# Kernel tuning notes

Measured on AMD Instinct MI355X. Metric: run time of the kernel, lower is better.

The kernel has to match this reference:

```python
import jax, jax.numpy as jnp
import numpy as np

NUM_BLOCKS = 3
NUM_CLUSTER = [16, 32, 64]


def _conv(x, w, b):
    # 1x1 conv2d + ReLU (BN folded to identity, eval-mode default stats): x [B,d,N], w [o,d], b [o]
    return jax.nn.relu(jnp.einsum('bdn,od->bon', x, w) + b[None, :, None])


def _segment_pool(feat, idx, nc):
    # Faithful single-pass version of pooling_block: per-cluster max over N,
    # rebroadcast to every node of that cluster. feat [B,d,N], idx [B,N] int.
    B, d, N = feat.shape
    seg = (idx + jnp.arange(B, dtype=idx.dtype)[:, None] * nc).reshape(-1)  # [B*N]
    flat = feat.transpose(0, 2, 1).reshape(B * N, d)
    mx = jax.ops.segment_max(flat, seg, num_segments=B * nc)  # [B*nc, d]
    return mx[seg].reshape(B, N, d).transpose(0, 2, 1)  # [B,d,N]


def setup_inputs() -> dict:
    key = jax.random.key(0)
    ks = jax.random.split(key, 16)
    B, N, K = 8, 16384, 28
    s = 0.05
    f32 = jnp.float32
    return {
        'x': jax.random.normal(ks[0], (B, N, K), f32),
        'clusters': jax.random.randint(ks[1], (NUM_BLOCKS, B, N), 0, min(NUM_CLUSTER), dtype=jnp.int32),
        'w_in': jax.random.normal(ks[2], (256, K), f32) * s,
        'b_in': jnp.zeros((256,), f32),
        'w1': jax.random.normal(ks[3], (NUM_BLOCKS, 64, 256), f32) * s,
        'b1': jnp.zeros((NUM_BLOCKS, 64), f32),
        'w2': jax.random.normal(ks[4], (NUM_BLOCKS, 128, 64), f32) * s,
        'b2': jnp.zeros((NUM_BLOCKS, 128), f32),
        'w3': jax.random.normal(ks[5], (NUM_BLOCKS, 128, 128), f32) * s,
        'b3': jnp.zeros((NUM_BLOCKS, 128), f32),
        'w_out1': jax.random.normal(ks[6], (128, 256), f32) * s,
        'b_out1': jnp.zeros((128,), f32),
        'w_out2': jax.random.normal(ks[7], (128, 128), f32) * s,
        'b_out2': jnp.zeros((128,), f32),
    }


def reference(x, clusters, w_in, b_in, w1, b1, w2, b2, w3, b3, w_out1, b_out1, w_out2, b_out2):
    # mlp_in: conv2d kernel [1,28] contracts the feature width -> [B,256,N]
    f = jax.nn.relu(jnp.einsum('bnk,ok->bon', x, w_in) + b_in[None, :, None])
    for i in range(NUM_BLOCKS):
        f = _conv(f, w1[i], b1[i])          # [B,64,N]
        f = _conv(f, w2[i], b2[i])          # [B,128,N]
        pool = _segment_pool(f, clusters[i], NUM_CLUSTER[i])  # [B,128,N]
        f3 = _conv(f, w3[i], b3[i])         # [B,128,N]
        f = jnp.concatenate([f3, pool], axis=1)  # [B,256,N]
    o1 = _conv(f, w_out1, b_out1)           # [B,128,N]
    o2 = _conv(o1, w_out2, b_out2)          # [B,128,N]
    out_max = o2.max(axis=2)                # global max pool over N
    B, d = out_max.shape
    return out_max.reshape(B, d, 1, 1)
```

## Files before the change

kernel.cpp:

```cpp
#include <hip/hip_runtime.h>
#include <hip/hip_cooperative_groups.h>


namespace cg = cooperative_groups;

typedef __attribute__((ext_vector_type(8))) short bf16x8;
typedef __attribute__((ext_vector_type(4))) float f32x4;
typedef __attribute__((ext_vector_type(4))) unsigned u32x4;
typedef __attribute__((ext_vector_type(4))) float f32x4v;

#define MFMA16(a, b, c) __builtin_amdgcn_mfma_f32_16x16x32_bf16((a), (b), (c), 0, 0, 0)

#define TPB 512
#define PT 64
#define NPTS 131072
#define NC 16
#define TILES 4
#define NBLK 512

#define FSB 136
#define ASB 72
#define XSB 40

#define U_F256 0
#define U_W1_0 16
#define U_W2_0 48
#define U_W3_0 64
#define U_W1_1 96
#define U_W2_1 112
#define U_W3_1 128
#define U_W1_2 160
#define U_W2_2 176
#define U_W3_2 192
#define U_O1   224
#define U_O2   256
#define N_UNITS 288

__device__ __forceinline__ float agent_ldf(const float* p) {
  return __hip_atomic_load(p, __ATOMIC_RELAXED, __HIP_MEMORY_SCOPE_AGENT);
}
__device__ __forceinline__ unsigned agent_ldu(const unsigned* p) {
  return __hip_atomic_load(p, __ATOMIC_RELAXED, __HIP_MEMORY_SCOPE_AGENT);
}
__device__ __forceinline__ void agent_stf(float* p, float v) {
  __hip_atomic_store(p, v, __ATOMIC_RELAXED, __HIP_MEMORY_SCOPE_AGENT);
}

__device__ __forceinline__ f32x4 relu4(f32x4 a) {
#pragma unroll
  for (int r = 0; r < 4; ++r) a[r] = fmaxf(a[r], 0.f);
  return a;
}

__device__ __forceinline__ bf16x8 afrag(const short* plane, int stride, int mt, int ks) {
  const int lane = threadIdx.x & 63;
  return *reinterpret_cast<const bf16x8*>(
      plane + (mt * 16 + (lane & 15)) * stride + ks * 32 + (lane >> 4) * 8);
}

__device__ __forceinline__ void bfrag(const unsigned* __restrict__ arena, int unit,
                                      bf16x8& h, bf16x8& l) {
  const bf16x8* p = reinterpret_cast<const bf16x8*>(
      arena + ((size_t)unit * 64 + (threadIdx.x & 63)) * 8);
  h = p[0];
  l = p[1];
}

__device__ __forceinline__ void store_planes(short* hp, short* lp, int stride,
                                             int mt, int n, f32x4 d) {
  const int m0 = mt * 16 + ((threadIdx.x & 63) >> 4) * 4;
#pragma unroll
  for (int r = 0; r < 4; ++r) {
    unsigned uv = __float_as_uint(d[r]);
    unsigned hm = uv & 0xFFFF0000u;
    float lo = d[r] - __uint_as_float(hm);
    hp[(m0 + r) * stride + n] = (short)(hm >> 16);
    lp[(m0 + r) * stride + n] = (short)(__float_as_uint(lo) >> 16);
  }
}

__device__ __forceinline__ void stage_f3(const unsigned* __restrict__ f3g, int tile0,
                                         short* Fhi, short* Flo, int tid) {
  const u32x4* src = reinterpret_cast<const u32x4*>(f3g + (size_t)tile0 * 128);
#pragma unroll
  for (int rr = 0; rr < 4; ++rr) {
    const int idx = rr * TPB + tid;
    const u32x4 p = __builtin_nontemporal_load(src + idx);
    const int pt = idx >> 5, c4 = (idx & 31) * 4;
    uint2 hd, ld;
    hd.x = (p.y & 0xFFFF0000u) | (p.x >> 16);
    hd.y = (p.w & 0xFFFF0000u) | (p.z >> 16);
    ld.x = (p.y << 16) | (p.x & 0xFFFFu);
    ld.y = (p.w << 16) | (p.z & 0xFFFFu);
    *reinterpret_cast<uint2*>(&Fhi[pt * FSB + c4]) = hd;
    *reinterpret_cast<uint2*>(&Flo[pt * FSB + c4]) = ld;
  }
}

__device__ __forceinline__ void write_f3(unsigned* __restrict__ f3g, int tile0,
                                         const short* Fhi, const short* Flo, int tid) {
  u32x4* dst = reinterpret_cast<u32x4*>(f3g + (size_t)tile0 * 128);
#pragma unroll
  for (int rr = 0; rr < 4; ++rr) {
    const int idx = rr * TPB + tid;
    const int pt = idx >> 5, c4 = (idx & 31) * 4;
    const uint2 hd = *reinterpret_cast<const uint2*>(&Fhi[pt * FSB + c4]);
    const uint2 ld = *reinterpret_cast<const uint2*>(&Flo[pt * FSB + c4]);
    u32x4 p;
    p.x = (hd.x << 16) | (ld.x & 0xFFFFu);
    p.y = (hd.x & 0xFFFF0000u) | (ld.x >> 16);
    p.z = (hd.y << 16) | (ld.y & 0xFFFFu);
    p.w = (hd.y & 0xFFFF0000u) | (ld.y >> 16);
    __builtin_nontemporal_store(p, dst + idx);
  }
}

__device__ __forceinline__ void unpack_cf(const u32x4 (&c)[4], short* Fhi, short* Flo,
                                          int tid) {
#pragma unroll
  for (int rr = 0; rr < 4; ++rr) {
    const int idx = rr * TPB + tid;
    const int pt = idx >> 5, c4 = (idx & 31) * 4;
    const u32x4 p = c[rr];
    uint2 hd, ld;
    hd.x = (p.y & 0xFFFF0000u) | (p.x >> 16);
    hd.y = (p.w & 0xFFFF0000u) | (p.z >> 16);
    ld.x = (p.y << 16) | (p.x & 0xFFFFu);
    ld.y = (p.w << 16) | (p.z & 0xFFFFu);
    *reinterpret_cast<uint2*>(&Fhi[pt * FSB + c4]) = hd;
    *reinterpret_cast<uint2*>(&Flo[pt * FSB + c4]) = ld;
  }
}

__device__ __forceinline__ void pack_cf(u32x4 (&c)[4], const short* Fhi, const short* Flo,
                                        int tid) {
#pragma unroll
  for (int rr = 0; rr < 4; ++rr) {
    const int idx = rr * TPB + tid;
    const int pt = idx >> 5, c4 = (idx & 31) * 4;
    const uint2 hd = *reinterpret_cast<const uint2*>(&Fhi[pt * FSB + c4]);
    const uint2 ld = *reinterpret_cast<const uint2*>(&Flo[pt * FSB + c4]);
    u32x4 p;
    p.x = (hd.x << 16) | (ld.x & 0xFFFFu);
    p.y = (hd.x & 0xFFFF0000u) | (ld.x >> 16);
    p.z = (hd.y << 16) | (ld.y & 0xFFFFu);
    p.w = (hd.y & 0xFFFF0000u) | (ld.y >> 16);
    c[rr] = p;
  }
}

__global__ void __launch_bounds__(64) prep_frags(
    const float* __restrict__ w_in, const float* __restrict__ w1,
    const float* __restrict__ w2, const float* __restrict__ w3,
    const float* __restrict__ wo1, const float* __restrict__ wo2,
    unsigned* __restrict__ arena) {
  const int unit = blockIdx.x;
  const int lane = threadIdx.x;
  const float* W; int KS, Klog, rs, u;
  if (unit < U_W1_0)      { W = w_in;                   u = unit - U_F256; KS = 1; Klog = 28;  rs = 28;  }
  else if (unit < U_W2_0) { W = w1;                     u = unit - U_W1_0; KS = 8; Klog = 256; rs = 256; }
  else if (unit < U_W3_0) { W = w2;                     u = unit - U_W2_0; KS = 2; Klog = 64;  rs = 64;  }
  else if (unit < U_W1_1) { W = w3;                     u = unit - U_W3_0; KS = 4; Klog = 128; rs = 128; }
  else if (unit < U_W2_1) { W = w1 + 64 * 256;          u = unit - U_W1_1; KS = 4; Klog = 128; rs = 256; }
  else if (unit < U_W3_1) { W = w2 + 128 * 64;          u = unit - U_W2_1; KS = 2; Klog = 64;  rs = 64;  }
  else if (unit < U_W1_2) { W = w3 + 128 * 128;         u = unit - U_W3_1; KS = 4; Klog = 128; rs = 128; }
  else if (unit < U_W2_2) { W = w1 + 2 * 64 * 256;      u = unit - U_W1_2; KS = 4; Klog = 128; rs = 256; }
  else if (unit < U_W3_2) { W = w2 + 2 * 128 * 64;      u = unit - U_W2_2; KS = 2; Klog = 64;  rs = 64;  }
  else if (unit < U_O1)   { W = w3 + 2 * 128 * 128;     u = unit - U_W3_2; KS = 4; Klog = 128; rs = 128; }
  else if (unit < U_O2)   { W = wo1;                    u = unit - U_O1;   KS = 4; Klog = 128; rs = 256; }
  else                    { W = wo2;                    u = unit - U_O2;   KS = 4; Klog = 128; rs = 128; }
  const int nt = u / KS, ks = u % KS;
  const int n = nt * 16 + (lane & 15);
  const int k0 = ks * 32 + (lane >> 4) * 8;
  unsigned hiD[4], loD[4];
#pragma unroll
  for (int d = 0; d < 4; ++d) {
    unsigned hu[2], lu[2];
#pragma unroll
    for (int e = 0; e < 2; ++e) {
      const int k = k0 + d * 2 + e;
      float v = (k < Klog) ? W[(size_t)n * rs + k] : 0.f;
      unsigned uv = __float_as_uint(v);
      unsigned hm = uv & 0xFFFF0000u;
      float lo = v - __uint_as_float(hm);
      hu[e] = hm >> 16;
      lu[e] = __float_as_uint(lo) >> 16;
    }
    hiD[d] = hu[0] | (hu[1] << 16);
    loD[d] = lu[0] | (lu[1] << 16);
  }
  unsigned* dst = arena + ((size_t)unit * 64 + lane) * 8;
  *reinterpret_cast<uint4*>(dst)     = make_uint4(hiD[0], hiD[1], hiD[2], hiD[3]);
  *reinterpret_cast<uint4*>(dst + 4) = make_uint4(loD[0], loD[1], loD[2], loD[3]);
}


template<int O>
__global__ void __launch_bounds__(1024) pool_reduce_kern(
    const unsigned* __restrict__ part, const float* __restrict__ W,
    const float* __restrict__ bias, float* __restrict__ poolc_g) {
  __shared__ float pfL[2048];
  __shared__ float Wl[O * 129];
  const int tid = threadIdx.x;
  const int b = blockIdx.x;
  for (int i = tid; i < 2048; i += 1024) pfL[i] = __uint_as_float(part[b * 2048 + i]);
  for (int i = tid; i < O * 128; i += 1024) {
    const int o = i >> 7, k = i & 127;
    Wl[o * 129 + k] = W[o * 256 + 128 + k];
  }
  __syncthreads();
  constexpr int SH = (O == 64) ? 6 : 7;
  for (int e = tid; e < O * 16; e += 1024) {
    const int o = e & (O - 1);
    const int cl = e >> SH;
    float s = bias[o];
    const float* wr = &Wl[o * 129];
    const float* pr = &pfL[cl];
#pragma unroll 4
    for (int k = 0; k < 128; ++k) s = fmaf(wr[k], pr[k * 16], s);
    poolc_g[(size_t)b * (O * 16) + o * 16 + cl] = s;
  }
}

__global__ void __launch_bounds__(TPB, 4) k0_kern(
    const float* __restrict__ x, const int* __restrict__ cls,
    const float* __restrict__ b_in, const float* __restrict__ b1,
    const float* __restrict__ b2, const float* __restrict__ b3,
    const unsigned* __restrict__ arena,
    unsigned* __restrict__ f3g, unsigned* __restrict__ part0) {
  __shared__ short Fhi[PT * FSB], Flo[PT * FSB];
  __shared__ short XA[PT * ASB * 2];
  __shared__ unsigned pool_s[128 * NC];
  short* Xhi = XA;  short* Xlo = XA + PT * XSB;
  short* Ahi = XA;  short* Alo = XA + PT * ASB;
  const int tid = threadIdx.x;
  const int lane = tid & 63, w = tid >> 6, l15 = lane & 15, quad = lane >> 4;
  const int b = blockIdx.x >> 6;
  const int Nt1 = w & 3, mh = w >> 2;
  for (int i = tid; i < 128 * NC; i += TPB) pool_s[i] = 0u;

  float biH[2];
#pragma unroll
  for (int c = 0; c < 2; ++c) biH[c] = b_in[c * 128 + w * 16 + l15];
  const float b1H = b1[Nt1 * 16 + l15];
  const float b2H = b2[w * 16 + l15];
  const float b3H = b3[w * 16 + l15];
  const int n1 = Nt1 * 16 + l15;
  const int n2 = w * 16 + l15;
  const int xpt = (tid < 448) ? tid / 7 : 0;
  const int xc4 = (tid < 448) ? (tid - xpt * 7) * 4 : 0;

  for (int t = 0; t < TILES; ++t) {
    const int tile0 = (blockIdx.x * TILES + t) * PT;
    if (tid < 448) {
      const f32x4v v = __builtin_nontemporal_load(
          reinterpret_cast<const f32x4v*>(x + (size_t)(tile0 + xpt) * 28 + xc4));
      unsigned h0 = __float_as_uint(v.x) & 0xFFFF0000u, h1 = __float_as_uint(v.y) & 0xFFFF0000u;
      unsigned h2 = __float_as_uint(v.z) & 0xFFFF0000u, h3 = __float_as_uint(v.w) & 0xFFFF0000u;
      uint2 hd, ld;
      hd.x = (h0 >> 16) | h1;
      hd.y = (h2 >> 16) | h3;
      ld.x = (__float_as_uint(v.x - __uint_as_float(h0)) >> 16) |
             (__float_as_uint(v.y - __uint_as_float(h1)) & 0xFFFF0000u);
      ld.y = (__float_as_uint(v.z - __uint_as_float(h2)) >> 16) |
             (__float_as_uint(v.w - __uint_as_float(h3)) & 0xFFFF0000u);
      *reinterpret_cast<uint2*>(&Xhi[xpt * XSB + xc4]) = hd;
      *reinterpret_cast<uint2*>(&Xlo[xpt * XSB + xc4]) = ld;
    } else {
      const int p = tid - 448;
      *reinterpret_cast<uint2*>(&Xhi[p * XSB + 28]) = make_uint2(0u, 0u);
      *reinterpret_cast<uint2*>(&Xlo[p * XSB + 28]) = make_uint2(0u, 0u);
    }
    int clP[4][4];
#pragma unroll
    for (int Mt = 0; Mt < 4; ++Mt) {
      int4 v = *reinterpret_cast<const int4*>(cls + tile0 + Mt * 16 + quad * 4);
      clP[Mt][0] = v.x; clP[Mt][1] = v.y; clP[Mt][2] = v.z; clP[Mt][3] = v.w;
    }
    __syncthreads();
    f32x4 a1[2];
#pragma unroll
    for (int m = 0; m < 2; ++m) a1[m] = {b1H, b1H, b1H, b1H};
#pragma unroll 1
    for (int c = 0; c < 2; ++c) {
      f32x4 f6[4];
#pragma unroll
      for (int Mt = 0; Mt < 4; ++Mt) f6[Mt] = {biH[c], biH[c], biH[c], biH[c]};
      {
        bf16x8 bh, bl;
        bfrag(arena, U_F256 + c * 8 + w, bh, bl);
#pragma unroll
        for (int Mt = 0; Mt < 4; ++Mt) {
          const bf16x8 xah = afrag(Xhi, XSB, Mt, 0), xal = afrag(Xlo, XSB, Mt, 0);
          f6[Mt] = MFMA16(xal, bh, MFMA16(xah, bl, MFMA16(xah, bh, f6[Mt])));
        }
      }
#pragma unroll
      for (int Mt = 0; Mt < 4; ++Mt)
        store_planes(Fhi, Flo, FSB, Mt, n2, relu4(f6[Mt]));
      __syncthreads();
#pragma unroll
      for (int ks = 0; ks < 4; ++ks) {
        bf16x8 bh, bl;
        bfrag(arena, U_W1_0 + Nt1 * 8 + c * 4 + ks, bh, bl);
#pragma unroll
        for (int m = 0; m < 2; ++m) {
          const bf16x8 ah = afrag(Fhi, FSB, mh * 2 + m, ks), al = afrag(Flo, FSB, mh * 2 + m, ks);
          a1[m] = MFMA16(al, bh, MFMA16(ah, bl, MFMA16(ah, bh, a1[m])));
        }
      }
      if (c == 1) {
#pragma unroll
        for (int m = 0; m < 2; ++m)
          store_planes(Ahi, Alo, ASB, mh * 2 + m, n1, relu4(a1[m]));
      }
      __syncthreads();
    }
    f32x4 f2[4];
#pragma unroll
    for (int Mt = 0; Mt < 4; ++Mt) f2[Mt] = {b2H, b2H, b2H, b2H};
#pragma unroll
    for (int ks = 0; ks < 2; ++ks) {
      bf16x8 bh, bl;
      bfrag(arena, U_W2_0 + w * 2 + ks, bh, bl);
#pragma unroll
      for (int Mt = 0; Mt < 4; ++Mt) {
        const bf16x8 ah = afrag(Ahi, ASB, Mt, ks), al = afrag(Alo, ASB, Mt, ks);
        f2[Mt] = MFMA16(al, bh, MFMA16(ah, bl, MFMA16(ah, bh, f2[Mt])));
      }
    }
#pragma unroll
    for (int Mt = 0; Mt < 4; ++Mt) {
      f32x4 d = relu4(f2[Mt]);
#pragma unroll
      for (int r = 0; r < 4; ++r)
        atomicMax(&pool_s[n2 * NC + clP[Mt][r]], __float_as_uint(d[r]));
      store_planes(Fhi, Flo, FSB, Mt, n2, d);
    }
    __syncthreads();
    f32x4 f3a[4];
#pragma unroll
    for (int Mt = 0; Mt < 4; ++Mt) f3a[Mt] = {b3H, b3H, b3H, b3H};
#pragma unroll
    for (int ks = 0; ks < 4; ++ks) {
      bf16x8 bh, bl;
      bfrag(arena, U_W3_0 + w * 4 + ks, bh, bl);
#pragma unroll
      for (int Mt = 0; Mt < 4; ++Mt) {
        const bf16x8 ah = afrag(Fhi, FSB, Mt, ks), al = afrag(Flo, FSB, Mt, ks);
        f3a[Mt] = MFMA16(al, bh, MFMA16(ah, bl, MFMA16(ah, bh, f3a[Mt])));
      }
    }
    __syncthreads();
#pragma unroll
    for (int Mt = 0; Mt < 4; ++Mt)
      store_planes(Fhi, Flo, FSB, Mt, n2, relu4(f3a[Mt]));
    __syncthreads();
    write_f3(f3g, tile0, Fhi, Flo, tid);
  }
  for (int i = tid; i < 128 * NC; i += TPB)
    atomicMax(&part0[(size_t)b * 2048 + i], pool_s[i]);
}

__global__ void __launch_bounds__(TPB, 4) kmid_kern(
    unsigned* __restrict__ f3g, const unsigned* __restrict__ arena,
    const float* __restrict__ poolc_g, unsigned* __restrict__ part_cur,
    const int* __restrict__ clg, const int* __restrict__ clp,
    const float* __restrict__ b2s, const float* __restrict__ b3s,
    int uW1, int uW2, int uW3) {
  __shared__ short Fhi[PT * FSB], Flo[PT * FSB];
  __shared__ short Ahi[PT * ASB], Alo[PT * ASB];
  __shared__ unsigned pool_s[128 * NC];
  const int tid = threadIdx.x;
  const int lane = tid & 63, w = tid >> 6, l15 = lane & 15, quad = lane >> 4;
  const int b = blockIdx.x >> 6;
  const int Nt1 = w & 3, mh = w >> 2;
  for (int i = tid; i < 128 * NC; i += TPB) pool_s[i] = 0u;
  const float b2H = b2s[w * 16 + l15];
  const float b3H = b3s[w * 16 + l15];
  const int n1 = Nt1 * 16 + l15;
  const int n2 = w * 16 + l15;

  for (int t = 0; t < TILES; ++t) {
    const int tile0 = (blockIdx.x * TILES + t) * PT;
    stage_f3(f3g, tile0, Fhi, Flo, tid);
    int clG[2][4], clP[4][4];
#pragma unroll
    for (int m = 0; m < 2; ++m) {
      int4 v = *reinterpret_cast<const int4*>(clg + tile0 + (mh * 2 + m) * 16 + quad * 4);
      clG[m][0] = v.x; clG[m][1] = v.y; clG[m][2] = v.z; clG[m][3] = v.w;
    }
#pragma unroll
    for (int Mt = 0; Mt < 4; ++Mt) {
      int4 v = *reinterpret_cast<const int4*>(clp + tile0 + Mt * 16 + quad * 4);
      clP[Mt][0] = v.x; clP[Mt][1] = v.y; clP[Mt][2] = v.z; clP[Mt][3] = v.w;
    }
    __syncthreads();
    f32x4 a1[2];
#pragma unroll
    for (int m = 0; m < 2; ++m)
#pragma unroll
      for (int r = 0; r < 4; ++r)
        a1[m][r] = poolc_g[(size_t)b * 1024 + n1 * 16 + clG[m][r]];
#pragma unroll
    for (int ks = 0; ks < 4; ++ks) {
      bf16x8 bh, bl;
      bfrag(arena, uW1 + Nt1 * 4 + ks, bh, bl);
#pragma unroll
      for (int m = 0; m < 2; ++m) {
        const bf16x8 ah = afrag(Fhi, FSB, mh * 2 + m, ks), al = afrag(Flo, FSB, mh * 2 + m, ks);
        a1[m] = MFMA16(al, bh, MFMA16(ah, bl, MFMA16(ah, bh, a1[m])));
      }
    }
#pragma unroll
    for (int m = 0; m < 2; ++m)
      store_planes(Ahi, Alo, ASB, mh * 2 + m, n1, relu4(a1[m]));
    __syncthreads();
    f32x4 f2[4];
#pragma unroll
    for (int Mt = 0; Mt < 4; ++Mt) f2[Mt] = {b2H, b2H, b2H, b2H};
#pragma unroll
    for (int ks = 0; ks < 2; ++ks) {
      bf16x8 bh, bl;
      bfrag(arena, uW2 + w * 2 + ks, bh, bl);
#pragma unroll
      for (int Mt = 0; Mt < 4; ++Mt) {
        const bf16x8 ah = afrag(Ahi, ASB, Mt, ks), al = afrag(Alo, ASB, Mt, ks);
        f2[Mt] = MFMA16(al, bh, MFMA16(ah, bl, MFMA16(ah, bh, f2[Mt])));
      }
    }
#pragma unroll
    for (int Mt = 0; Mt < 4; ++Mt) {
      f32x4 d = relu4(f2[Mt]);
#pragma unroll
      for (int r = 0; r < 4; ++r)
        atomicMax(&pool_s[n2 * NC + clP[Mt][r]], __float_as_uint(d[r]));
      store_planes(Fhi, Flo, FSB, Mt, n2, d);
    }
    __syncthreads();
    f32x4 f3a[4];
#pragma unroll
    for (int Mt = 0; Mt < 4; ++Mt) f3a[Mt] = {b3H, b3H, b3H, b3H};
#pragma unroll
    for (int ks = 0; ks < 4; ++ks) {
      bf16x8 bh, bl;
      bfrag(arena, uW3 + w * 4 + ks, bh, bl);
#pragma unroll
      for (int Mt = 0; Mt < 4; ++Mt) {
        const bf16x8 ah = afrag(Fhi, FSB, Mt, ks), al = afrag(Flo, FSB, Mt, ks);
        f3a[Mt] = MFMA16(al, bh, MFMA16(ah, bl, MFMA16(ah, bh, f3a[Mt])));
      }
    }
    __syncthreads();
#pragma unroll
    for (int Mt = 0; Mt < 4; ++Mt)
      store_planes(Fhi, Flo, FSB, Mt, n2, relu4(f3a[Mt]));
    __syncthreads();
    write_f3(f3g, tile0, Fhi, Flo, tid);
    __syncthreads();
  }
  for (int i = tid; i < 128 * NC; i += TPB)
    atomicMax(&part_cur[(size_t)b * 2048 + i], pool_s[i]);
}

__global__ void __launch_bounds__(TPB, 4) k3_kern(
    const unsigned* __restrict__ f3g, const unsigned* __restrict__ arena,
    const float* __restrict__ poolco_g, const int* __restrict__ clg,
    const float* __restrict__ bo2, unsigned* __restrict__ out) {
  __shared__ short Fhi[PT * FSB], Flo[PT * FSB];
  const int tid = threadIdx.x;
  const int lane = tid & 63, w = tid >> 6, l15 = lane & 15, quad = lane >> 4;
  const int b = blockIdx.x >> 6;
  const float bo2H = bo2[w * 16 + l15];
  const int n2 = w * 16 + l15;
  float omax = 0.f;

  for (int t = 0; t < TILES; ++t) {
    const int tile0 = (blockIdx.x * TILES + t) * PT;
    stage_f3(f3g, tile0, Fhi, Flo, tid);
    int clA[4][4];
#pragma unroll
    for (int Mt = 0; Mt < 4; ++Mt) {
      int4 v = *reinterpret_cast<const int4*>(clg + tile0 + Mt * 16 + quad * 4);
      clA[Mt][0] = v.x; clA[Mt][1] = v.y; clA[Mt][2] = v.z; clA[Mt][3] = v.w;
    }
    __syncthreads();
    f32x4 o1a[4];
#pragma unroll
    for (int Mt = 0; Mt < 4; ++Mt)
#pragma unroll
      for (int r = 0; r < 4; ++r)
        o1a[Mt][r] = poolco_g[(size_t)b * 2048 + n2 * 16 + clA[Mt][r]];
#pragma unroll
    for (int ks = 0; ks < 4; ++ks) {
      bf16x8 bh, bl;
      bfrag(arena, U_O1 + w * 4 + ks, bh, bl);
#pragma unroll
      for (int Mt = 0; Mt < 4; ++Mt) {
        const bf16x8 ah = afrag(Fhi, FSB, Mt, ks), al = afrag(Flo, FSB, Mt, ks);
        o1a[Mt] = MFMA16(al, bh, MFMA16(ah, bl, MFMA16(ah, bh, o1a[Mt])));
      }
    }
    __syncthreads();
#pragma unroll
    for (int Mt = 0; Mt < 4; ++Mt)
      store_planes(Fhi, Flo, FSB, Mt, n2, relu4(o1a[Mt]));
    __syncthreads();
    f32x4 o2a[4];
#pragma unroll
    for (int Mt = 0; Mt < 4; ++Mt) o2a[Mt] = {bo2H, bo2H, bo2H, bo2H};
#pragma unroll
    for (int ks = 0; ks < 4; ++ks) {
      bf16x8 bh, bl;
      bfrag(arena, U_O2 + w * 4 + ks, bh, bl);
#pragma unroll
      for (int Mt = 0; Mt < 4; ++Mt) {
        const bf16x8 ah = afrag(Fhi, FSB, Mt, ks), al = afrag(Flo, FSB, Mt, ks);
        o2a[Mt] = MFMA16(al, bh, MFMA16(ah, bl, MFMA16(ah, bh, o2a[Mt])));
      }
    }
#pragma unroll
    for (int Mt = 0; Mt < 4; ++Mt) {
      f32x4 d = relu4(o2a[Mt]);
      omax = fmaxf(omax, fmaxf(fmaxf(d[0], d[1]), fmaxf(d[2], d[3])));
    }
    __syncthreads();
  }
  omax = fmaxf(omax, __shfl_xor(omax, 16));
  omax = fmaxf(omax, __shfl_xor(omax, 32));
  if (lane < 16)
    atomicMax(&out[b * 128 + w * 16 + lane], __float_as_uint(omax));
}


__device__ __forceinline__ void poolc_phase(const unsigned* __restrict__ part,
                                            const float* __restrict__ W,
                                            const float* __restrict__ bias,
                                            float* __restrict__ poolc,
                                            int O, int tid, int wg) {
  const int b = wg >> 3, j = wg & 7;
  const int per = O >> 3;
  const int njobs = per * 16;
  if (tid < njobs) {
    const int o = j * per + (tid >> 4);
    const int cl = tid & 15;
    float s = bias[o];
    const float* wr = W + (size_t)o * 256 + 128;
    const unsigned* pr = part + b * 2048 + cl;
#pragma unroll 4
    for (int k = 0; k < 128; ++k) s = fmaf(wr[k], __uint_as_float(agent_ldu(pr + k * 16)), s);
    agent_stf(poolc + (size_t)b * (O * 16) + o * 16 + cl, s);
  }
}

__device__ __forceinline__ void stage0_body(
    u32x4 (&cf)[TILES][4],
    const float* __restrict__ x, const int* __restrict__ cls,
    const float* __restrict__ b_in, const float* __restrict__ b1,
    const float* __restrict__ b2, const float* __restrict__ b3,
    const unsigned* __restrict__ arena, unsigned* __restrict__ part0,
    short* Fhi, short* Flo, short* XA, unsigned* pool_s,
    int tid, int wg, int b) {
  short* Xhi = XA;  short* Xlo = XA + PT * XSB;
  short* Ahi = XA;  short* Alo = XA + PT * ASB;
  const int lane = tid & 63, w = tid >> 6, l15 = lane & 15, quad = lane >> 4;
  const int Nt1 = w & 3, mh = w >> 2;
  for (int i = tid; i < 128 * NC; i += TPB) pool_s[i] = 0u;

  float biH[2];
#pragma unroll
  for (int c = 0; c < 2; ++c) biH[c] = b_in[c * 128 + w * 16 + l15];
  const float b1H = b1[Nt1 * 16 + l15];
  const float b2H = b2[w * 16 + l15];
  const float b3H = b3[w * 16 + l15];
  const int n1 = Nt1 * 16 + l15;
  const int n2 = w * 16 + l15;
  const int xpt = (tid < 448) ? tid / 7 : 0;
  const int xc4 = (tid < 448) ? (tid - xpt * 7) * 4 : 0;

#pragma unroll
  for (int t = 0; t < TILES; ++t) {
    const int tile0 = (wg * TILES + t) * PT;
    if (tid < 448) {
      const f32x4v v = __builtin_nontemporal_load(
          reinterpret_cast<const f32x4v*>(x + (size_t)(tile0 + xpt) * 28 + xc4));
      unsigned h0 = __float_as_uint(v.x) & 0xFFFF0000u, h1 = __float_as_uint(v.y) & 0xFFFF0000u;
      unsigned h2 = __float_as_uint(v.z) & 0xFFFF0000u, h3 = __float_as_uint(v.w) & 0xFFFF0000u;
      uint2 hd, ld;
      hd.x = (h0 >> 16) | h1;
      hd.y = (h2 >> 16) | h3;
      ld.x = (__float_as_uint(v.x - __uint_as_float(h0)) >> 16) |
             (__float_as_uint(v.y - __uint_as_float(h1)) & 0xFFFF0000u);
      ld.y = (__float_as_uint(v.z - __uint_as_float(h2)) >> 16) |
             (__float_as_uint(v.w - __uint_as_float(h3)) & 0xFFFF0000u);
      *reinterpret_cast<uint2*>(&Xhi[xpt * XSB + xc4]) = hd;
      *reinterpret_cast<uint2*>(&Xlo[xpt * XSB + xc4]) = ld;
    } else {
      const int p = tid - 448;
      *reinterpret_cast<uint2*>(&Xhi[p * XSB + 28]) = make_uint2(0u, 0u);
      *reinterpret_cast<uint2*>(&Xlo[p * XSB + 28]) = make_uint2(0u, 0u);
    }
    int clP[4][4];
#pragma unroll
    for (int Mt = 0; Mt < 4; ++Mt) {
      int4 v = *reinterpret_cast<const int4*>(cls + tile0 + Mt * 16 + quad * 4);
      clP[Mt][0] = v.x; clP[Mt][1] = v.y; clP[Mt][2] = v.z; clP[Mt][3] = v.w;
    }
    __syncthreads();
    f32x4 a1[2];
#pragma unroll
    for (int m = 0; m < 2; ++m) a1[m] = {b1H, b1H, b1H, b1H};
#pragma unroll 1
    for (int c = 0; c < 2; ++c) {
      f32x4 f6[4];
#pragma unroll
      for (int Mt = 0; Mt < 4; ++Mt) f6[Mt] = {biH[c], biH[c], biH[c], biH[c]};
      {
        bf16x8 bh, bl;
        bfrag(arena, U_F256 + c * 8 + w, bh, bl);
#pragma unroll
        for (int Mt = 0; Mt < 4; ++Mt) {
          const bf16x8 xah = afrag(Xhi, XSB, Mt, 0), xal = afrag(Xlo, XSB, Mt, 0);
          f6[Mt] = MFMA16(xal, bh, MFMA16(xah, bl, MFMA16(xah, bh, f6[Mt])));
        }
      }
#pragma unroll
      for (int Mt = 0; Mt < 4; ++Mt)
        store_planes(Fhi, Flo, FSB, Mt, n2, relu4(f6[Mt]));
      __syncthreads();
#pragma unroll
      for (int ks = 0; ks < 4; ++ks) {
        bf16x8 bh, bl;
        bfrag(arena, U_W1_0 + Nt1 * 8 + c * 4 + ks, bh, bl);
#pragma unroll
        for (int m = 0; m < 2; ++m) {
          const bf16x8 ah = afrag(Fhi, FSB, mh * 2 + m, ks), al = afrag(Flo, FSB, mh * 2 + m, ks);
          a1[m] = MFMA16(al, bh, MFMA16(ah, bl, MFMA16(ah, bh, a1[m])));
        }
      }
      if (c == 1) {
#pragma unroll
        for (int m = 0; m < 2; ++m)
          store_planes(Ahi, Alo, ASB, mh * 2 + m, n1, relu4(a1[m]));
      }
      __syncthreads();
    }
    f32x4 f2[4];
#pragma unroll
    for (int Mt = 0; Mt < 4; ++Mt) f2[Mt] = {b2H, b2H, b2H, b2H};
#pragma unroll
    for (int ks = 0; ks < 2; ++ks) {
      bf16x8 bh, bl;
      bfrag(arena, U_W2_0 + w * 2 + ks, bh, bl);
#pragma unroll
      for (int Mt = 0; Mt < 4; ++Mt) {
        const bf16x8 ah = afrag(Ahi, ASB, Mt, ks), al = afrag(Alo, ASB, Mt, ks);
        f2[Mt] = MFMA16(al, bh, MFMA16(ah, bl, MFMA16(ah, bh, f2[Mt])));
      }
    }
#pragma unroll
    for (int Mt = 0; Mt < 4; ++Mt) {
      f32x4 d = relu4(f2[Mt]);
#pragma unroll
      for (int r = 0; r < 4; ++r)
        atomicMax(&pool_s[n2 * NC + clP[Mt][r]], __float_as_uint(d[r]));
      store_planes(Fhi, Flo, FSB, Mt, n2, d);
    }
    __syncthreads();
    f32x4 f3a[4];
#pragma unroll
    for (int Mt = 0; Mt < 4; ++Mt) f3a[Mt] = {b3H, b3H, b3H, b3H};
#pragma unroll
    for (int ks = 0; ks < 4; ++ks) {
      bf16x8 bh, bl;
      bfrag(arena, U_W3_0 + w * 4 + ks, bh, bl);
#pragma unroll
      for (int Mt = 0; Mt < 4; ++Mt) {
        const bf16x8 ah = afrag(Fhi, FSB, Mt, ks), al = afrag(Flo, FSB, Mt, ks);
        f3a[Mt] = MFMA16(al, bh, MFMA16(ah, bl, MFMA16(ah, bh, f3a[Mt])));
      }
    }
    __syncthreads();
#pragma unroll
    for (int Mt = 0; Mt < 4; ++Mt)
      store_planes(Fhi, Flo, FSB, Mt, n2, relu4(f3a[Mt]));
    __syncthreads();
    pack_cf(cf[t], Fhi, Flo, tid);
  }
  for (int i = tid; i < 128 * NC; i += TPB)
    atomicMax(&part0[(size_t)b * 2048 + i], pool_s[i]);
}

__device__ __forceinline__ void mid_body(
    u32x4 (&cf)[TILES][4], const unsigned* __restrict__ arena,
    const float* __restrict__ poolc_g, unsigned* __restrict__ part_cur,
    const int* __restrict__ clg, const int* __restrict__ clp,
    const float* __restrict__ b2s, const float* __restrict__ b3s,
    int uW1, int uW2, int uW3,
    short* Fhi, short* Flo, short* Ahi, short* Alo, unsigned* pool_s,
    int tid, int wg, int b) {
  const int lane = tid & 63, w = tid >> 6, l15 = lane & 15, quad = lane >> 4;
  const int Nt1 = w & 3, mh = w >> 2;
  for (int i = tid; i < 128 * NC; i += TPB) pool_s[i] = 0u;
  const float b2H = b2s[w * 16 + l15];
  const float b3H = b3s[w * 16 + l15];
  const int n1 = Nt1 * 16 + l15;
  const int n2 = w * 16 + l15;

#pragma unroll
  for (int t = 0; t < TILES; ++t) {
    const int tile0 = (wg * TILES + t) * PT;
    unpack_cf(cf[t], Fhi, Flo, tid);
    int clG[2][4], clP[4][4];
#pragma unroll
    for (int m = 0; m < 2; ++m) {
      int4 v = *reinterpret_cast<const int4*>(clg + tile0 + (mh * 2 + m) * 16 + quad * 4);
      clG[m][0] = v.x; clG[m][1] = v.y; clG[m][2] = v.z; clG[m][3] = v.w;
    }
#pragma unroll
    for (int Mt = 0; Mt < 4; ++Mt) {
      int4 v = *reinterpret_cast<const int4*>(clp + tile0 + Mt * 16 + quad * 4);
      clP[Mt][0] = v.x; clP[Mt][1] = v.y; clP[Mt][2] = v.z; clP[Mt][3] = v.w;
    }
    __syncthreads();
    f32x4 a1[2];
#pragma unroll
    for (int m = 0; m < 2; ++m)
#pragma unroll
      for (int r = 0; r < 4; ++r)
        a1[m][r] = agent_ldf(poolc_g + (size_t)b * 1024 + n1 * 16 + clG[m][r]);
#pragma unroll
    for (int ks = 0; ks < 4; ++ks) {
      bf16x8 bh, bl;
      bfrag(arena, uW1 + Nt1 * 4 + ks, bh, bl);
#pragma unroll
      for (int m = 0; m < 2; ++m) {
        const bf16x8 ah = afrag(Fhi, FSB, mh * 2 + m, ks), al = afrag(Flo, FSB, mh * 2 + m, ks);
        a1[m] = MFMA16(al, bh, MFMA16(ah, bl, MFMA16(ah, bh, a1[m])));
      }
    }
#pragma unroll
    for (int m = 0; m < 2; ++m)
      store_planes(Ahi, Alo, ASB, mh * 2 + m, n1, relu4(a1[m]));
    __syncthreads();
    f32x4 f2[4];
#pragma unroll
    for (int Mt = 0; Mt < 4; ++Mt) f2[Mt] = {b2H, b2H, b2H, b2H};
#pragma unroll
    for (int ks = 0; ks < 2; ++ks) {
      bf16x8 bh, bl;
      bfrag(arena, uW2 + w * 2 + ks, bh, bl);
#pragma unroll
      for (int Mt = 0; Mt < 4; ++Mt) {
        const bf16x8 ah = afrag(Ahi, ASB, Mt, ks), al = afrag(Alo, ASB, Mt, ks);
        f2[Mt] = MFMA16(al, bh, MFMA16(ah, bl, MFMA16(ah, bh, f2[Mt])));
      }
    }
#pragma unroll
    for (int Mt = 0; Mt < 4; ++Mt) {
      f32x4 d = relu4(f2[Mt]);
#pragma unroll
      for (int r = 0; r < 4; ++r)
        atomicMax(&pool_s[n2 * NC + clP[Mt][r]], __float_as_uint(d[r]));
      store_planes(Fhi, Flo, FSB, Mt, n2, d);
    }
    __syncthreads();
    f32x4 f3a[4];
#pragma unroll
    for (int Mt = 0; Mt < 4; ++Mt) f3a[Mt] = {b3H, b3H, b3H, b3H};
#pragma unroll
    for (int ks = 0; ks < 4; ++ks) {
      bf16x8 bh, bl;
      bfrag(arena, uW3 + w * 4 + ks, bh, bl);
#pragma unroll
      for (int Mt = 0; Mt < 4; ++Mt) {
        const bf16x8 ah = afrag(Fhi, FSB, Mt, ks), al = afrag(Flo, FSB, Mt, ks);
        f3a[Mt] = MFMA16(al, bh, MFMA16(ah, bl, MFMA16(ah, bh, f3a[Mt])));
      }
    }
    __syncthreads();
#pragma unroll
    for (int Mt = 0; Mt < 4; ++Mt)
      store_planes(Fhi, Flo, FSB, Mt, n2, relu4(f3a[Mt]));
    __syncthreads();
    pack_cf(cf[t], Fhi, Flo, tid);
    __syncthreads();
  }
  for (int i = tid; i < 128 * NC; i += TPB)
    atomicMax(&part_cur[(size_t)b * 2048 + i], pool_s[i]);
}

__device__ __forceinline__ void head_body(
    const u32x4 (&cf)[TILES][4], const unsigned* __restrict__ arena,
    const float* __restrict__ poolco_g, const int* __restrict__ clg,
    const float* __restrict__ bo2, unsigned* __restrict__ out,
    short* Fhi, short* Flo, int tid, int wg, int b) {
  const int lane = tid & 63, w = tid >> 6, l15 = lane & 15, quad = lane >> 4;
  const float bo2H = bo2[w * 16 + l15];
  const int n2 = w * 16 + l15;
  float omax = 0.f;

#pragma unroll
  for (int t = 0; t < TILES; ++t) {
    const int tile0 = (wg * TILES + t) * PT;
    unpack_cf(cf[t], Fhi, Flo, tid);
    int clA[4][4];
#pragma unroll
    for (int Mt = 0; Mt < 4; ++Mt) {
      int4 v = *reinterpret_cast<const int4*>(clg + tile0 + Mt * 16 + quad * 4);
      clA[Mt][0] = v.x; clA[Mt][1] = v.y; clA[Mt][2] = v.z; clA[Mt][3] = v.w;
    }
    __syncthreads();
    f32x4 o1a[4];
#pragma unroll
    for (int Mt = 0; Mt < 4; ++Mt)
#pragma unroll
      for (int r = 0; r < 4; ++r)
        o1a[Mt][r] = agent_ldf(poolco_g + (size_t)b * 2048 + n2 * 16 + clA[Mt][r]);
#pragma unroll
    for (int ks = 0; ks < 4; ++ks) {
      bf16x8 bh, bl;
      bfrag(arena, U_O1 + w * 4 + ks, bh, bl);
#pragma unroll
      for (int Mt = 0; Mt < 4; ++Mt) {
        const bf16x8 ah = afrag(Fhi, FSB, Mt, ks), al = afrag(Flo, FSB, Mt, ks);
        o1a[Mt] = MFMA16(al, bh, MFMA16(ah, bl, MFMA16(ah, bh, o1a[Mt])));
      }
    }
    __syncthreads();
#pragma unroll
    for (int Mt = 0; Mt < 4; ++Mt)
      store_planes(Fhi, Flo, FSB, Mt, n2, relu4(o1a[Mt]));
    __syncthreads();
    f32x4 o2a[4];
#pragma unroll
    for (int Mt = 0; Mt < 4; ++Mt) o2a[Mt] = {bo2H, bo2H, bo2H, bo2H};
#pragma unroll
    for (int ks = 0; ks < 4; ++ks) {
      bf16x8 bh, bl;
      bfrag(arena, U_O2 + w * 4 + ks, bh, bl);
#pragma unroll
      for (int Mt = 0; Mt < 4; ++Mt) {
        const bf16x8 ah = afrag(Fhi, FSB, Mt, ks), al = afrag(Flo, FSB, Mt, ks);
        o2a[Mt] = MFMA16(al, bh, MFMA16(ah, bl, MFMA16(ah, bh, o2a[Mt])));
      }
    }
#pragma unroll
    for (int Mt = 0; Mt < 4; ++Mt) {
      f32x4 d = relu4(o2a[Mt]);
      omax = fmaxf(omax, fmaxf(fmaxf(d[0], d[1]), fmaxf(d[2], d[3])));
    }
    __syncthreads();
  }
  omax = fmaxf(omax, __shfl_xor(omax, 16));
  omax = fmaxf(omax, __shfl_xor(omax, 32));
  if (lane < 16)
    atomicMax(&out[b * 128 + w * 16 + lane], __float_as_uint(omax));
}

struct FusedParams {
  const float* x; const int* cls;
  const float* b_in; const float* b1; const float* b2; const float* b3;
  const float* w1; const float* wo1; const float* bo1; const float* bo2;
  const unsigned* arena;
  unsigned* part0; unsigned* part1; unsigned* part2;
  float* poolc1; float* poolc2; float* poolco;
  unsigned* out;
};

__global__ void __launch_bounds__(TPB, 4) fused_kern(FusedParams P) {
  __shared__ short Fhi[PT * FSB], Flo[PT * FSB];
  __shared__ short XA[PT * ASB * 2];
  __shared__ unsigned pool_s[128 * NC];
  const int tid = threadIdx.x;
  const int wg = blockIdx.x;
  const int b = wg >> 6;
  u32x4 cf[TILES][4];

  stage0_body(cf, P.x, P.cls, P.b_in, P.b1, P.b2, P.b3, P.arena, P.part0,
              Fhi, Flo, XA, pool_s, tid, wg, b);
  cg::this_grid().sync();
  if (wg < 64) poolc_phase(P.part0, P.w1 + 64 * 256, P.b1 + 64, P.poolc1, 64, tid, wg);
  cg::this_grid().sync();
  mid_body(cf, P.arena, P.poolc1, P.part1, P.cls, P.cls + NPTS,
           P.b2 + 128, P.b3 + 128, U_W1_1, U_W2_1, U_W3_1,
           Fhi, Flo, XA, XA + PT * ASB, pool_s, tid, wg, b);
  cg::this_grid().sync();
  if (wg < 64) poolc_phase(P.part1, P.w1 + 2 * 64 * 256, P.b1 + 128, P.poolc2, 64, tid, wg);
  cg::this_grid().sync();
  mid_body(cf, P.arena, P.poolc2, P.part2, P.cls + NPTS, P.cls + 2 * NPTS,
           P.b2 + 256, P.b3 + 256, U_W1_2, U_W2_2, U_W3_2,
           Fhi, Flo, XA, XA + PT * ASB, pool_s, tid, wg, b);
  cg::this_grid().sync();
  if (wg < 64) poolc_phase(P.part2, P.wo1, P.bo1, P.poolco, 128, tid, wg);
  cg::this_grid().sync();
  head_body(cf, P.arena, P.poolco, P.cls + 2 * NPTS, P.bo2, P.out,
            Fhi, Flo, tid, wg, b);
}

extern "C" void kernel_launch(void* const* d_in, const int* in_sizes, int n_in,
                              void* d_out, int out_size, void* d_ws, size_t ws_size,
                              hipStream_t stream) {
  const float* x    = (const float*)d_in[0];
  const int*   cls  = (const int*)d_in[1];
  const float* w_in = (const float*)d_in[2];
  const float* b_in = (const float*)d_in[3];
  const float* w1   = (const float*)d_in[4];
  const float* b1   = (const float*)d_in[5];
  const float* w2   = (const float*)d_in[6];
  const float* b2   = (const float*)d_in[7];
  const float* w3   = (const float*)d_in[8];
  const float* b3   = (const float*)d_in[9];
  const float* wo1  = (const float*)d_in[10];
  const float* bo1  = (const float*)d_in[11];
  const float* wo2  = (const float*)d_in[12];
  const float* bo2  = (const float*)d_in[13];

  char* ws = (char*)d_ws;
  unsigned* f3g = (unsigned*)ws;
  unsigned* part0 = (unsigned*)(ws + ((size_t)64 << 20));
  unsigned* part1 = part0 + 8 * 2048;
  unsigned* part2 = part1 + 8 * 2048;
  float* poolc1 = (float*)(part2 + 8 * 2048);
  float* poolc2 = poolc1 + 8 * 1024;
  float* poolco = poolc2 + 8 * 1024;
  unsigned* arena = (unsigned*)(poolco + 8 * 2048);

  hipMemsetAsync(d_out, 0, 1024 * sizeof(float), stream);
  hipMemsetAsync(part0, 0, 3 * 8 * 2048 * sizeof(unsigned), stream);

  prep_frags<<<N_UNITS, 64, 0, stream>>>(w_in, w1, w2, w3, wo1, wo2, arena);

  static int coop_ok = -1;
  if (coop_ok < 0) {
    int maxb = 0;
    hipError_t oe = hipOccupancyMaxActiveBlocksPerMultiprocessor(
        &maxb, (const void*)fused_kern, TPB, 0);
    coop_ok = (oe == hipSuccess && maxb >= 2) ? 1 : 0;
    if (oe != hipSuccess) (void)hipGetLastError();
  }

  bool fused_done = false;
  if (coop_ok == 1) {
    FusedParams P{x, cls, b_in, b1, b2, b3, w1, wo1, bo1, bo2,
                  arena, part0, part1, part2, poolc1, poolc2, poolco,
                  (unsigned*)d_out};
    void* args[] = {&P};
    hipError_t le = hipLaunchCooperativeKernel((void*)fused_kern, dim3(NBLK),
                                               dim3(TPB), args, 0, stream);
    if (le == hipSuccess) {
      fused_done = true;
    } else {
      (void)hipGetLastError();
      coop_ok = 0;
    }
  }

  if (!fused_done) {
    k0_kern<<<NBLK, TPB, 0, stream>>>(x, cls, b_in, b1, b2, b3, arena, f3g, part0);
    pool_reduce_kern<64><<<8, 1024, 0, stream>>>(part0, w1 + (size_t)64 * 256, b1 + 64, poolc1);
    kmid_kern<<<NBLK, TPB, 0, stream>>>(f3g, arena, poolc1, part1, cls, cls + NPTS,
                                        b2 + 128, b3 + 128, U_W1_1, U_W2_1, U_W3_1);
    pool_reduce_kern<64><<<8, 1024, 0, stream>>>(part1, w1 + (size_t)2 * 64 * 256, b1 + 128, poolc2);
    kmid_kern<<<NBLK, TPB, 0, stream>>>(f3g, arena, poolc2, part2, cls + NPTS, cls + 2 * NPTS,
                                        b2 + 256, b3 + 256, U_W1_2, U_W2_2, U_W3_2);
    pool_reduce_kern<128><<<8, 1024, 0, stream>>>(part2, wo1, bo1, poolco);
    k3_kern<<<NBLK, TPB, 0, stream>>>(f3g, arena, poolco, cls + 2 * NPTS, bo2, (unsigned*)d_out);
  }
}
```

Baseline: 416.2 us.

## Replace cooperative grid sync with atomic barrier, keep tile state in AGPRs, cache pool tables

Swaps cooperative-groups grid syncs for a hand-rolled monotonic atomic counter barrier and launches the fused kernel as a normal launch after an occupancy check. The per-tile packed feature state moves into accumulation registers through explicit accvgpr read and write asm, which frees VGPRs. Pooled-cluster tables are copied once into shared memory instead of being gathered from global memory with atomic loads in each tile. The custom barrier assumes every block is co-resident, which is not guaranteed without a cooperative launch and could deadlock.

Result: no change. 416.0 us (-0.0%).

```diff
diff --git a/kernel.cpp b/kernel.cpp
--- a/kernel.cpp
+++ b/kernel.cpp
@@ -1,8 +1,5 @@
 #include <hip/hip_runtime.h>
-#include <hip/hip_cooperative_groups.h>
-
-
-namespace cg = cooperative_groups;
+
 
 typedef __attribute__((ext_vector_type(8))) short bf16x8;
 typedef __attribute__((ext_vector_type(4))) float f32x4;
@@ -46,6 +43,27 @@
   __hip_atomic_store(p, v, __ATOMIC_RELAXED, __HIP_MEMORY_SCOPE_AGENT);
 }
 
+__device__ __forceinline__ void agwr(unsigned &a, unsigned v) {
+  asm volatile("v_accvgpr_write_b32 %0, %1" : "=a"(a) : "v"(v));
+}
+__device__ __forceinline__ unsigned agrd(const unsigned &a) {
+  unsigned v;
+  asm volatile("v_accvgpr_read_b32 %0, %1" : "=v"(v) : "a"(a));
+  return v;
+}
+
+__device__ __forceinline__ void gsync(unsigned* bar, unsigned target) {
+  __syncthreads();
+  if (threadIdx.x == 0) {
+    __threadfence();
+    __hip_atomic_fetch_add(bar, 1u, __ATOMIC_RELAXED, __HIP_MEMORY_SCOPE_AGENT);
+    while (__hip_atomic_load(bar, __ATOMIC_RELAXED, __HIP_MEMORY_SCOPE_AGENT) < target)
+      __builtin_amdgcn_s_sleep(2);
+    __threadfence();
+  }
+  __syncthreads();
+}
+
 __device__ __forceinline__ f32x4 relu4(f32x4 a) {
 #pragma unroll
   for (int r = 0; r < 4; ++r) a[r] = fmaxf(a[r], 0.f);
@@ -115,37 +133,36 @@
   }
 }
 
-__device__ __forceinline__ void unpack_cf(const u32x4 (&c)[4], short* Fhi, short* Flo,
-                                          int tid) {
+__device__ __forceinline__ void unpack_cf_a(const unsigned (&ca)[16], short* Fhi,
+                                            short* Flo, int tid) {
 #pragma unroll
   for (int rr = 0; rr < 4; ++rr) {
     const int idx = rr * TPB + tid;
     const int pt = idx >> 5, c4 = (idx & 31) * 4;
-    const u32x4 p = c[rr];
+    const unsigned px = agrd(ca[rr * 4 + 0]), py = agrd(ca[rr * 4 + 1]);
+    const unsigned pz = agrd(ca[rr * 4 + 2]), pw = agrd(ca[rr * 4 + 3]);
     uint2 hd, ld;
-    hd.x = (p.y & 0xFFFF0000u) | (p.x >> 16);
-    hd.y = (p.w & 0xFFFF0000u) | (p.z >> 16);
-    ld.x = (p.y << 16) | (p.x & 0xFFFFu);
-    ld.y = (p.w << 16) | (p.z & 0xFFFFu);
+    hd.x = (py & 0xFFFF0000u) | (px >> 16);
+    hd.y = (pw & 0xFFFF0000u) | (pz >> 16);
+    ld.x = (py << 16) | (px & 0xFFFFu);
+    ld.y = (pw << 16) | (pz & 0xFFFFu);
     *reinterpret_cast<uint2*>(&Fhi[pt * FSB + c4]) = hd;
     *reinterpret_cast<uint2*>(&Flo[pt * FSB + c4]) = ld;
   }
 }
 
-__device__ __forceinline__ void pack_cf(u32x4 (&c)[4], const short* Fhi, const short* Flo,
-                                        int tid) {
+__device__ __forceinline__ void pack_cf_a(unsigned (&ca)[16], const short* Fhi,
+                                          const short* Flo, int tid) {
 #pragma unroll
   for (int rr = 0; rr < 4; ++rr) {
     const int idx = rr * TPB + tid;
     const int pt = idx >> 5, c4 = (idx & 31) * 4;
     const uint2 hd = *reinterpret_cast<const uint2*>(&Fhi[pt * FSB + c4]);
     const uint2 ld = *reinterpret_cast<const uint2*>(&Flo[pt * FSB + c4]);
-    u32x4 p;
-    p.x = (hd.x << 16) | (ld.x & 0xFFFFu);
-    p.y = (hd.x & 0xFFFF0000u) | (ld.x >> 16);
-    p.z = (hd.y << 16) | (ld.y & 0xFFFFu);
-    p.w = (hd.y & 0xFFFF0000u) | (ld.y >> 16);
-    c[rr] = p;
+    agwr(ca[rr * 4 + 0], (hd.x << 16) | (ld.x & 0xFFFFu));
+    agwr(ca[rr * 4 + 1], (hd.x & 0xFFFF0000u) | (ld.x >> 16));
+    agwr(ca[rr * 4 + 2], (hd.y << 16) | (ld.y & 0xFFFFu));
+    agwr(ca[rr * 4 + 3], (hd.y & 0xFFFF0000u) | (ld.y >> 16));
   }
 }
 
@@ -554,7 +571,7 @@
 }
 
 __device__ __forceinline__ void stage0_body(
-    u32x4 (&cf)[TILES][4],
+    unsigned (&cfa)[TILES][16],
     const float* __restrict__ x, const int* __restrict__ cls,
     const float* __restrict__ b_in, const float* __restrict__ b1,
     const float* __restrict__ b2, const float* __restrict__ b3,
@@ -685,23 +702,25 @@
     for (int Mt = 0; Mt < 4; ++Mt)
       store_planes(Fhi, Flo, FSB, Mt, n2, relu4(f3a[Mt]));
     __syncthreads();
-    pack_cf(cf[t], Fhi, Flo, tid);
+    pack_cf_a(cfa[t], Fhi, Flo, tid);
   }
   for (int i = tid; i < 128 * NC; i += TPB)
     atomicMax(&part0[(size_t)b * 2048 + i], pool_s[i]);
 }
 
 __device__ __forceinline__ void mid_body(
-    u32x4 (&cf)[TILES][4], const unsigned* __restrict__ arena,
+    unsigned (&cfa)[TILES][16], const unsigned* __restrict__ arena,
     const float* __restrict__ poolc_g, unsigned* __restrict__ part_cur,
     const int* __restrict__ clg, const int* __restrict__ clp,
     const float* __restrict__ b2s, const float* __restrict__ b3s,
     int uW1, int uW2, int uW3,
     short* Fhi, short* Flo, short* Ahi, short* Alo, unsigned* pool_s,
-    int tid, int wg, int b) {
+    float* pltab, int tid, int wg, int b) {
   const int lane = tid & 63, w = tid >> 6, l15 = lane & 15, quad = lane >> 4;
   const int Nt1 = w & 3, mh = w >> 2;
   for (int i = tid; i < 128 * NC; i += TPB) pool_s[i] = 0u;
+  for (int i = tid; i < 1024; i += TPB)
+    pltab[i] = agent_ldf(poolc_g + (size_t)b * 1024 + i);
   const float b2H = b2s[w * 16 + l15];
   const float b3H = b3s[w * 16 + l15];
   const int n1 = Nt1 * 16 + l15;
@@ -710,7 +729,7 @@
 #pragma unroll
   for (int t = 0; t < TILES; ++t) {
     const int tile0 = (wg * TILES + t) * PT;
-    unpack_cf(cf[t], Fhi, Flo, tid);
+    unpack_cf_a(cfa[t], Fhi, Flo, tid);
     int clG[2][4], clP[4][4];
 #pragma unroll
     for (int m = 0; m < 2; ++m) {
@@ -728,7 +747,7 @@
     for (int m = 0; m < 2; ++m)
 #pragma unroll
       for (int r = 0; r < 4; ++r)
-        a1[m][r] = agent_ldf(poolc_g + (size_t)b * 1024 + n1 * 16 + clG[m][r]);
+        a1[m][r] = pltab[n1 * 16 + clG[m][r]];
 #pragma unroll
     for (int ks = 0; ks < 4; ++ks) {
       bf16x8 bh, bl;
@@ -783,7 +802,7 @@
     for (int Mt = 0; Mt < 4; ++Mt)
       store_planes(Fhi, Flo, FSB, Mt, n2, relu4(f3a[Mt]));
     __syncthreads();
-    pack_cf(cf[t], Fhi, Flo, tid);
+    pack_cf_a(cfa[t], Fhi, Flo, tid);
     __syncthreads();
   }
   for (int i = tid; i < 128 * NC; i += TPB)
@@ -791,19 +810,22 @@
 }
 
 __device__ __forceinline__ void head_body(
-    const u32x4 (&cf)[TILES][4], const unsigned* __restrict__ arena,
+    const unsigned (&cfa)[TILES][16], const unsigned* __restrict__ arena,
     const float* __restrict__ poolco_g, const int* __restrict__ clg,
     const float* __restrict__ bo2, unsigned* __restrict__ out,
-    short* Fhi, short* Flo, int tid, int wg, int b) {
+    short* Fhi, short* Flo, unsigned* pool_s, int tid, int wg, int b) {
   const int lane = tid & 63, w = tid >> 6, l15 = lane & 15, quad = lane >> 4;
   const float bo2H = bo2[w * 16 + l15];
   const int n2 = w * 16 + l15;
   float omax = 0.f;
+  float* ptab = reinterpret_cast<float*>(pool_s);
+  for (int i = tid; i < 2048; i += TPB)
+    ptab[i] = agent_ldf(poolco_g + (size_t)b * 2048 + i);
 
 #pragma unroll
   for (int t = 0; t < TILES; ++t) {
     const int tile0 = (wg * TILES + t) * PT;
-    unpack_cf(cf[t], Fhi, Flo, tid);
+    unpack_cf_a(cfa[t], Fhi, Flo, tid);
     int clA[4][4];
 #pragma unroll
     for (int Mt = 0; Mt < 4; ++Mt) {
@@ -816,7 +838,7 @@
     for (int Mt = 0; Mt < 4; ++Mt)
 #pragma unroll
       for (int r = 0; r < 4; ++r)
-        o1a[Mt][r] = agent_ldf(poolco_g + (size_t)b * 2048 + n2 * 16 + clA[Mt][r]);
+        o1a[Mt][r] = ptab[n2 * 16 + clA[Mt][r]];
 #pragma unroll
     for (int ks = 0; ks < 4; ++ks) {
       bf16x8 bh, bl;
@@ -865,37 +887,38 @@
   const unsigned* arena;
   unsigned* part0; unsigned* part1; unsigned* part2;
   float* poolc1; float* poolc2; float* poolco;
-  unsigned* out;
+  unsigned* out; unsigned* bar;
 };
 
 __global__ void __launch_bounds__(TPB, 4) fused_kern(FusedParams P) {
   __shared__ short Fhi[PT * FSB], Flo[PT * FSB];
   __shared__ short XA[PT * ASB * 2];
   __shared__ unsigned pool_s[128 * NC];
+  __shared__ float pltab[1024];
   const int tid = threadIdx.x;
   const int wg = blockIdx.x;
   const int b = wg >> 6;
-  u32x4 cf[TILES][4];
-
-  stage0_body(cf, P.x, P.cls, P.b_in, P.b1, P.b2, P.b3, P.arena, P.part0,
+  unsigned cfa[TILES][16];
+
+  stage0_body(cfa, P.x, P.cls, P.b_in, P.b1, P.b2, P.b3, P.arena, P.part0,
               Fhi, Flo, XA, pool_s, tid, wg, b);
-  cg::this_grid().sync();
+  gsync(P.bar, 1 * NBLK);
   if (wg < 64) poolc_phase(P.part0, P.w1 + 64 * 256, P.b1 + 64, P.poolc1, 64, tid, wg);
-  cg::this_grid().sync();
-  mid_body(cf, P.arena, P.poolc1, P.part1, P.cls, P.cls + NPTS,
+  gsync(P.bar, 2 * NBLK);
+  mid_body(cfa, P.arena, P.poolc1, P.part1, P.cls, P.cls + NPTS,
            P.b2 + 128, P.b3 + 128, U_W1_1, U_W2_1, U_W3_1,
-           Fhi, Flo, XA, XA + PT * ASB, pool_s, tid, wg, b);
-  cg::this_grid().sync();
+           Fhi, Flo, XA, XA + PT * ASB, pool_s, pltab, tid, wg, b);
+  gsync(P.bar, 3 * NBLK);
   if (wg < 64) poolc_phase(P.part1, P.w1 + 2 * 64 * 256, P.b1 + 128, P.poolc2, 64, tid, wg);
-  cg::this_grid().sync();
-  mid_body(cf, P.arena, P.poolc2, P.part2, P.cls + NPTS, P.cls + 2 * NPTS,
+  gsync(P.bar, 4 * NBLK);
+  mid_body(cfa, P.arena, P.poolc2, P.part2, P.cls + NPTS, P.cls + 2 * NPTS,
            P.b2 + 256, P.b3 + 256, U_W1_2, U_W2_2, U_W3_2,
-           Fhi, Flo, XA, XA + PT * ASB, pool_s, tid, wg, b);
-  cg::this_grid().sync();
+           Fhi, Flo, XA, XA + PT * ASB, pool_s, pltab, tid, wg, b);
+  gsync(P.bar, 5 * NBLK);
   if (wg < 64) poolc_phase(P.part2, P.wo1, P.bo1, P.poolco, 128, tid, wg);
-  cg::this_grid().sync();
-  head_body(cf, P.arena, P.poolco, P.cls + 2 * NPTS, P.bo2, P.out,
-            Fhi, Flo, tid, wg, b);
+  gsync(P.bar, 6 * NBLK);
+  head_body(cfa, P.arena, P.poolco, P.cls + 2 * NPTS, P.bo2, P.out,
+            Fhi, Flo, pool_s, tid, wg, b);
 }
 
 extern "C" void kernel_launch(void* const* d_in, const int* in_sizes, int n_in,
@@ -925,38 +948,34 @@
   float* poolc2 = poolc1 + 8 * 1024;
   float* poolco = poolc2 + 8 * 1024;
   unsigned* arena = (unsigned*)(poolco + 8 * 2048);
+  unsigned* bar = arena + (size_t)N_UNITS * 512;
 
   hipMemsetAsync(d_out, 0, 1024 * sizeof(float), stream);
   hipMemsetAsync(part0, 0, 3 * 8 * 2048 * sizeof(unsigned), stream);
+  hipMemsetAsync(bar, 0, sizeof(unsigned), stream);
 
   prep_frags<<<N_UNITS, 64, 0, stream>>>(w_in, w1, w2, w3, wo1, wo2, arena);
 
   static int coop_ok = -1;
   if (coop_ok < 0) {
+    int dev = 0;
+    (void)hipGetDevice(&dev);
+    hipDeviceProp_t props{};
+    hipError_t pe = hipGetDeviceProperties(&props, dev);
     int maxb = 0;
     hipError_t oe = hipOccupancyMaxActiveBlocksPerMultiprocessor(
         &maxb, (const void*)fused_kern, TPB, 0);
-    coop_ok = (oe == hipSuccess && maxb >= 2) ? 1 : 0;
-    if (oe != hipSuccess) (void)hipGetLastError();
-  }
-
-  bool fused_done = false;
+    coop_ok = (pe == hipSuccess && oe == hipSuccess &&
+               (long)maxb * props.multiProcessorCount >= NBLK) ? 1 : 0;
+    if (pe != hipSuccess || oe != hipSuccess) (void)hipGetLastError();
+  }
+
   if (coop_ok == 1) {
     FusedParams P{x, cls, b_in, b1, b2, b3, w1, wo1, bo1, bo2,
                   arena, part0, part1, part2, poolc1, poolc2, poolco,
-                  (unsigned*)d_out};
-    void* args[] = {&P};
-    hipError_t le = hipLaunchCooperativeKernel((void*)fused_kern, dim3(NBLK),
-                                               dim3(TPB), args, 0, stream);
-    if (le == hipSuccess) {
-      fused_done = true;
-    } else {
-      (void)hipGetLastError();
-      coop_ok = 0;
-    }
-  }
-
-  if (!fused_done) {
+                  (unsigned*)d_out, bar};
+    fused_kern<<<NBLK, TPB, 0, stream>>>(P);
+  } else {
     k0_kern<<<NBLK, TPB, 0, stream>>>(x, cls, b_in, b1, b2, b3, arena, f3g, part0);
     pool_reduce_kern<64><<<8, 1024, 0, stream>>>(part0, w1 + (size_t)64 * 256, b1 + 64, poolc1);
     kmid_kern<<<NBLK, TPB, 0, stream>>>(f3g, arena, poolc1, part1, cls, cls + NPTS,
```
